# Optimization experiments

Measured on AMD Instinct MI355X. Metric: run time of the kernel, lower is better.

## Reference

```python
import jax, jax.numpy as jnp
import numpy as np

D_MODEL = 512
NUM_HEADS = 8
D_K = D_MODEL // NUM_HEADS
B, L = 2, 4096


def setup_inputs() -> dict:
    key = jax.random.key(0)
    ks = jax.random.split(key, 11)
    s = 1.0 / np.sqrt(D_MODEL)
    return {
        "Q": jax.random.normal(ks[0], (B, L, D_MODEL), jnp.float32),
        "K": jax.random.normal(ks[1], (B, L, D_MODEL), jnp.float32),
        "V": jax.random.normal(ks[2], (B, L, D_MODEL), jnp.float32),
        "Wq": jax.random.normal(ks[3], (D_MODEL, D_MODEL), jnp.float32) * s,
        "bq": jax.random.normal(ks[4], (D_MODEL,), jnp.float32) * s,
        "Wk": jax.random.normal(ks[5], (D_MODEL, D_MODEL), jnp.float32) * s,
        "bk": jax.random.normal(ks[6], (D_MODEL,), jnp.float32) * s,
        "Wv": jax.random.normal(ks[7], (D_MODEL, D_MODEL), jnp.float32) * s,
        "bv": jax.random.normal(ks[8], (D_MODEL,), jnp.float32) * s,
        "Wo": jax.random.normal(ks[9], (D_MODEL, D_MODEL), jnp.float32) * s,
        "bo": jax.random.normal(ks[10], (D_MODEL,), jnp.float32) * s,
    }


def reference(Q, K, V, Wq, bq, Wk, bk, Wv, bv, Wo, bo):
    b, l, d = Q.shape
    h, dk = NUM_HEADS, D_K
    # projections: [B, L, D] -> [B, H, L, dk]
    def proj(x, W, bias):
        y = x @ W.T + bias
        return y.reshape(b, l, h, dk).transpose(0, 2, 1, 3)
    q = proj(Q, Wq, bq)
    k = proj(K, Wk, bk)
    v = proj(V, Wv, bv)
    scores = jnp.einsum("bhqd,bhkd->bhqk", q, k) / jnp.sqrt(jnp.float32(dk))
    attn = jax.nn.softmax(scores, axis=-1)
    head_out = jnp.einsum("bhqk,bhkd->bhqd", attn, v)
    out = head_out.transpose(0, 2, 1, 3).reshape(b, l, d)
    return out @ Wo.T + bo
```

## Files before the change

### kernel.cpp

```cpp
#include <hip/hip_runtime.h>
#include <hip/hip_bf16.h>

#define SEQ 4096
#define DM 512
#define DK 64
#define NT (SEQ / 64)

typedef __attribute__((ext_vector_type(8))) short bf16x8;
typedef __attribute__((ext_vector_type(4))) short bf16x4;
typedef __attribute__((ext_vector_type(4))) float f32x4;

#define QSCL 0.18033688011112043f

static __device__ __forceinline__ short bf16h(float f) {
    union { __hip_bfloat16 h; short s; } u;
    u.h = __float2bfloat16(f);
    return u.s;
}

static __device__ __forceinline__ float fexp2(float x) {
#if __has_builtin(__builtin_amdgcn_exp2f)
    return __builtin_amdgcn_exp2f(x);
#else
    return exp2f(x);
#endif
}

static __device__ __forceinline__ void cvt16(const float* __restrict__ p, short* dst) {
    float4 a = *(const float4*)p;
    float4 b = *(const float4*)(p + 4);
    float4 e = *(const float4*)(p + 8);
    float4 d = *(const float4*)(p + 12);
    bf16x8 x0, x1;
    x0[0] = bf16h(a.x); x0[1] = bf16h(a.y); x0[2] = bf16h(a.z); x0[3] = bf16h(a.w);
    x0[4] = bf16h(b.x); x0[5] = bf16h(b.y); x0[6] = bf16h(b.z); x0[7] = bf16h(b.w);
    x1[0] = bf16h(e.x); x1[1] = bf16h(e.y); x1[2] = bf16h(e.z); x1[3] = bf16h(e.w);
    x1[4] = bf16h(d.x); x1[5] = bf16h(d.y); x1[6] = bf16h(d.z); x1[7] = bf16h(d.w);
    *(bf16x8*)dst = x0;
    *(bf16x8*)(dst + 8) = x1;
}

__global__ __launch_bounds__(256) void proj_qkv(
        const float* __restrict__ Qx, const float* __restrict__ Kx, const float* __restrict__ Vx,
        const float* __restrict__ Wq, const float* __restrict__ Wk, const float* __restrict__ Wv,
        const float* __restrict__ bq, const float* __restrict__ bk, const float* __restrict__ bv,
        short* __restrict__ qo, short* __restrict__ ko, short* __restrict__ vo) {
    __shared__ short Xs[64][72];
    __shared__ short Ws[64][72];
    const int z = blockIdx.z;
    const float* X    = z == 0 ? Qx : z == 1 ? Kx : Vx;
    const float* W    = z == 0 ? Wq : z == 1 ? Wk : Wv;
    const float* bias = z == 0 ? bq : z == 1 ? bk : bv;

    const int t = threadIdx.x, lane = t & 63, w = t >> 6;
    const int g = lane >> 4, c = lane & 15;
    const int sr = t >> 2, sc = t & 3;
    const int m0 = blockIdx.x << 6, n0 = blockIdx.y << 6;

    f32x4 acc[4] = {};
    const float* px = X + (size_t)(m0 + sr) * DM + sc * 16;
    const float* pw = W + (size_t)(n0 + sr) * DM + sc * 16;

    for (int k0 = 0; k0 < DM; k0 += 64) {
        cvt16(px, &Xs[sr][sc * 16]);
        cvt16(pw, &Ws[sr][sc * 16]);
        px += 64; pw += 64;
        __syncthreads();
        #pragma unroll
        for (int kc = 0; kc < 2; ++kc) {
            bf16x8 a8 = *(bf16x8*)&Xs[16 * w + c][32 * kc + 8 * g];
            #pragma unroll
            for (int f = 0; f < 4; ++f) {
                bf16x8 b8 = *(bf16x8*)&Ws[16 * f + c][32 * kc + 8 * g];
                acc[f] = __builtin_amdgcn_mfma_f32_16x16x32_bf16(a8, b8, acc[f], 0, 0, 0);
            }
        }
        __syncthreads();
    }

    float bs[4];
    #pragma unroll
    for (int f = 0; f < 4; ++f) bs[f] = bias[n0 + 16 * f + c];
    const int b = m0 >> 12, h = blockIdx.y;

    if (z == 0 || z == 1) {
        short* Yp = z == 0 ? qo : ko;
        const float scl = z == 0 ? QSCL : 1.0f;
        #pragma unroll
        for (int f = 0; f < 4; ++f) {
            #pragma unroll
            for (int r = 0; r < 4; ++r) {
                int m = m0 + 16 * w + 4 * g + r;
                Yp[((size_t)(b * 8 + h) * SEQ + (m & 4095)) * DK + 16 * f + c] =
                    bf16h((acc[f][r] + bs[f]) * scl);
            }
        }
    } else {
        short (&Ls)[64][72] = Xs;
        #pragma unroll
        for (int f = 0; f < 4; ++f) {
            #pragma unroll
            for (int r = 0; r < 4; ++r)
                Ls[16 * f + c][16 * w + 4 * g + r] = bf16h(acc[f][r] + bs[f]);
        }
        __syncthreads();
        bf16x8 r0 = *(bf16x8*)&Ls[sr][sc * 16];
        bf16x8 r1 = *(bf16x8*)&Ls[sr][sc * 16 + 8];
        short* dst = vo + ((size_t)(b * 8 + h) * DK + sr) * SEQ + (m0 & 4095) + sc * 16;
        *(bf16x8*)dst = r0;
        *(bf16x8*)(dst + 8) = r1;
    }
}

__global__ __launch_bounds__(256) void proj_out(const short* __restrict__ Xb,
        const float* __restrict__ W, const float* __restrict__ bias, float* __restrict__ Y) {
    __shared__ short Xs[64][72];
    __shared__ short Ws[64][72];
    const int t = threadIdx.x, lane = t & 63, w = t >> 6;
    const int g = lane >> 4, c = lane & 15;
    const int sr = t >> 2, sc = t & 3;
    const int m0 = blockIdx.x << 6, n0 = blockIdx.y << 6;

    f32x4 acc[4] = {};
    const short* px = Xb + (size_t)(m0 + sr) * DM + sc * 16;
    const float* pw = W + (size_t)(n0 + sr) * DM + sc * 16;

    for (int k0 = 0; k0 < DM; k0 += 64) {
        *(bf16x8*)&Xs[sr][sc * 16]     = *(const bf16x8*)px;
        *(bf16x8*)&Xs[sr][sc * 16 + 8] = *(const bf16x8*)(px + 8);
        cvt16(pw, &Ws[sr][sc * 16]);
        px += 64; pw += 64;
        __syncthreads();
        #pragma unroll
        for (int kc = 0; kc < 2; ++kc) {
            bf16x8 a8 = *(bf16x8*)&Xs[16 * w + c][32 * kc + 8 * g];
            #pragma unroll
            for (int f = 0; f < 4; ++f) {
                bf16x8 b8 = *(bf16x8*)&Ws[16 * f + c][32 * kc + 8 * g];
                acc[f] = __builtin_amdgcn_mfma_f32_16x16x32_bf16(a8, b8, acc[f], 0, 0, 0);
            }
        }
        __syncthreads();
    }

    #pragma unroll
    for (int f = 0; f < 4; ++f) {
        float bs = bias[n0 + 16 * f + c];
        #pragma unroll
        for (int r = 0; r < 4; ++r) {
            int m = m0 + 16 * w + 4 * g + r;
            Y[(size_t)m * DM + n0 + 16 * f + c] = acc[f][r] + bs;
        }
    }
}

__global__ __launch_bounds__(256) void attn_fwd(const short* __restrict__ qp,
        const short* __restrict__ kp, const short* __restrict__ vtp, short* __restrict__ ho) {
    __shared__ short Ks[64][72];
    __shared__ short Vts[64][76];
    const int t = threadIdx.x, lane = t & 63, w = t >> 6;
    const int g = lane >> 4, c = lane & 15;
    const int sr = t >> 2, sc = t & 3;
    const int q0 = blockIdx.x << 6, bh = blockIdx.y;

    const short* qrow = qp + ((size_t)bh * SEQ + q0 + 16 * w + c) * DK;
    const bf16x8 qf0 = *(const bf16x8*)(qrow + 8 * g);
    const bf16x8 qf1 = *(const bf16x8*)(qrow + 32 + 8 * g);

    f32x4 o4[4] = {};
    float m_run = -3.0e38f, l_run = 0.f;

    const short* kptr = kp + (size_t)bh * SEQ * DK + (size_t)sr * DK + sc * 16;
    const short* vptr = vtp + (size_t)bh * DK * SEQ + (size_t)sr * SEQ + sc * 16;
    bf16x8 kr0 = *(const bf16x8*)kptr;
    bf16x8 kr1 = *(const bf16x8*)(kptr + 8);
    bf16x8 vr0 = *(const bf16x8*)vptr;
    bf16x8 vr1 = *(const bf16x8*)(vptr + 8);

    for (int kt = 0; kt < NT; ++kt) {
        *(bf16x8*)&Ks[sr][sc * 16]     = kr0;
        *(bf16x8*)&Ks[sr][sc * 16 + 8] = kr1;
        {
            bf16x4 t0 = {vr0[0], vr0[1], vr0[2], vr0[3]};
            bf16x4 t1 = {vr0[4], vr0[5], vr0[6], vr0[7]};
            bf16x4 t2 = {vr1[0], vr1[1], vr1[2], vr1[3]};
            bf16x4 t3 = {vr1[4], vr1[5], vr1[6], vr1[7]};
            *(bf16x4*)&Vts[sr][sc * 16]      = t0;
            *(bf16x4*)&Vts[sr][sc * 16 + 4]  = t1;
            *(bf16x4*)&Vts[sr][sc * 16 + 8]  = t2;
            *(bf16x4*)&Vts[sr][sc * 16 + 12] = t3;
        }
        __syncthreads();
        if (kt + 1 < NT) {
            kptr += 64 * DK;
            vptr += 64;
            kr0 = *(const bf16x8*)kptr;
            kr1 = *(const bf16x8*)(kptr + 8);
            vr0 = *(const bf16x8*)vptr;
            vr1 = *(const bf16x8*)(vptr + 8);
        }

        f32x4 s4[4] = {};
        #pragma unroll
        for (int f = 0; f < 4; ++f) {
            bf16x8 a8 = *(bf16x8*)&Ks[16 * f + c][8 * g];
            s4[f] = __builtin_amdgcn_mfma_f32_16x16x32_bf16(a8, qf0, s4[f], 0, 0, 0);
        }
        #pragma unroll
        for (int f = 0; f < 4; ++f) {
            bf16x8 a8 = *(bf16x8*)&Ks[16 * f + c][32 + 8 * g];
            s4[f] = __builtin_amdgcn_mfma_f32_16x16x32_bf16(a8, qf1, s4[f], 0, 0, 0);
        }

        float pm = s4[0][0];
        #pragma unroll
        for (int f = 0; f < 4; ++f) {
            #pragma unroll
            for (int r = 0; r < 4; ++r) pm = fmaxf(pm, s4[f][r]);
        }
        pm = fmaxf(pm, __shfl_xor(pm, 16));
        pm = fmaxf(pm, __shfl_xor(pm, 32));

        if (__any(pm > m_run + 8.0f)) {
            float mnew  = fmaxf(m_run, pm);
            float alpha = fexp2(m_run - mnew);
            l_run *= alpha;
            #pragma unroll
            for (int fd = 0; fd < 4; ++fd) {
                #pragma unroll
                for (int r = 0; r < 4; ++r) o4[fd][r] *= alpha;
            }
            m_run = mnew;
        }

        float rs = 0.f;
        #pragma unroll
        for (int f = 0; f < 4; ++f) {
            #pragma unroll
            for (int r = 0; r < 4; ++r) {
                float p = fexp2(s4[f][r] - m_run);
                s4[f][r] = p;
                rs += p;
            }
        }
        rs += __shfl_xor(rs, 16);
        rs += __shfl_xor(rs, 32);
        l_run += rs;

        #pragma unroll
        for (int f = 0; f < 4; ++f) {
            bf16x4 pb = { bf16h(s4[f][0]), bf16h(s4[f][1]), bf16h(s4[f][2]), bf16h(s4[f][3]) };
            #pragma unroll
            for (int fd = 0; fd < 4; ++fd) {
                bf16x4 va = *(bf16x4*)&Vts[16 * fd + c][16 * f + 4 * g];
                o4[fd] = __builtin_amdgcn_mfma_f32_16x16x16bf16_1k(va, pb, o4[fd], 0, 0, 0);
            }
        }
        __syncthreads();
    }

    const float inv = 1.0f / l_run;
    short (&Ls)[64][72] = Ks;
    #pragma unroll
    for (int fd = 0; fd < 4; ++fd) {
        #pragma unroll
        for (int r = 0; r < 4; ++r)
            Ls[16 * w + c][16 * fd + 4 * g + r] = bf16h(o4[fd][r] * inv);
    }
    __syncthreads();
    const int b = bh >> 3, h = bh & 7;
    bf16x8 r0 = *(bf16x8*)&Ls[sr][sc * 16];
    bf16x8 r1 = *(bf16x8*)&Ls[sr][sc * 16 + 8];
    short* dst = ho + ((size_t)(b * SEQ + q0 + sr)) * DM + h * DK + sc * 16;
    *(bf16x8*)dst = r0;
    *(bf16x8*)(dst + 8) = r1;
}

extern "C" void kernel_launch(void* const* d_in, const int* in_sizes, int n_in,
                              void* d_out, int out_size, void* d_ws, size_t ws_size,
                              hipStream_t stream) {
    const float* Q  = (const float*)d_in[0];
    const float* K  = (const float*)d_in[1];
    const float* V  = (const float*)d_in[2];
    const float* Wq = (const float*)d_in[3];
    const float* bq = (const float*)d_in[4];
    const float* Wk = (const float*)d_in[5];
    const float* bk = (const float*)d_in[6];
    const float* Wv = (const float*)d_in[7];
    const float* bv = (const float*)d_in[8];
    const float* Wo = (const float*)d_in[9];
    const float* bo = (const float*)d_in[10];

    const size_t NIN = (size_t)2 * SEQ * DM;

    short* qws  = (short*)d_ws;
    short* kws  = qws + NIN;
    short* vtws = kws + NIN;
    short* hws  = vtws + NIN;

    proj_qkv<<<dim3(128, 8, 3), 256, 0, stream>>>(Q, K, V, Wq, Wk, Wv, bq, bk, bv,
                                                  qws, kws, vtws);
    attn_fwd<<<dim3(SEQ / 64, 16), 256, 0, stream>>>(qws, kws, vtws, hws);
    proj_out<<<dim3(128, 8), 256, 0, stream>>>(hws, Wo, bo, (float*)d_out);
}
```

Before: 293.0 us.

## Enlarge projection GEMM tiles to 128x128 and prefetch next K-slice into registers

Both projection kernels move from 64x64 tiles with 256 threads to 128x128 tiles with 512 threads, and each wave now computes a 64x32 sub-tile (4x2 MFMAs) to get more reuse per LDS load. The global loads for the next K slice are issued into registers before the current slice's MFMAs, overlapping memory latency with compute. The V-transpose epilogue is reworked for the wider tile. In exchange, the grid shrinks (768 and 256 blocks) and register pressure rises, which may reduce occupancy and leave CUs idle for proj_out.

```diff
diff --git a/kernel.cpp b/kernel.cpp
--- a/kernel.cpp
+++ b/kernel.cpp
@@ -26,11 +26,8 @@
 #endif
 }
 
-static __device__ __forceinline__ void cvt16(const float* __restrict__ p, short* dst) {
-    float4 a = *(const float4*)p;
-    float4 b = *(const float4*)(p + 4);
-    float4 e = *(const float4*)(p + 8);
-    float4 d = *(const float4*)(p + 12);
+static __device__ __forceinline__ void cvt16r(float4 a, float4 b, float4 e, float4 d,
+                                              short* dst) {
     bf16x8 x0, x1;
     x0[0] = bf16h(a.x); x0[1] = bf16h(a.y); x0[2] = bf16h(a.z); x0[3] = bf16h(a.w);
     x0[4] = bf16h(b.x); x0[5] = bf16h(b.y); x0[6] = bf16h(b.z); x0[7] = bf16h(b.w);
@@ -40,13 +37,14 @@
     *(bf16x8*)(dst + 8) = x1;
 }
 
-__global__ __launch_bounds__(256) void proj_qkv(
+__global__ __launch_bounds__(512) void proj_qkv(
         const float* __restrict__ Qx, const float* __restrict__ Kx, const float* __restrict__ Vx,
         const float* __restrict__ Wq, const float* __restrict__ Wk, const float* __restrict__ Wv,
         const float* __restrict__ bq, const float* __restrict__ bk, const float* __restrict__ bv,
         short* __restrict__ qo, short* __restrict__ ko, short* __restrict__ vo) {
-    __shared__ short Xs[64][72];
-    __shared__ short Ws[64][72];
+    __shared__ short lds[2][128][72];
+    short (*As)[72] = lds[0];
+    short (*Bs)[72] = lds[1];
     const int z = blockIdx.z;
     const float* X    = z == 0 ? Qx : z == 1 ? Kx : Vx;
     const float* W    = z == 0 ? Wq : z == 1 ? Wk : Wv;
@@ -54,103 +52,147 @@
 
     const int t = threadIdx.x, lane = t & 63, w = t >> 6;
     const int g = lane >> 4, c = lane & 15;
-    const int sr = t >> 2, sc = t & 3;
-    const int m0 = blockIdx.x << 6, n0 = blockIdx.y << 6;
-
-    f32x4 acc[4] = {};
-    const float* px = X + (size_t)(m0 + sr) * DM + sc * 16;
-    const float* pw = W + (size_t)(n0 + sr) * DM + sc * 16;
-
-    for (int k0 = 0; k0 < DM; k0 += 64) {
-        cvt16(px, &Xs[sr][sc * 16]);
-        cvt16(pw, &Ws[sr][sc * 16]);
-        px += 64; pw += 64;
-        __syncthreads();
+    const int wr = w >> 2, wc = w & 3;
+    const int row = t >> 2, sc = t & 3;
+    const int m0 = blockIdx.x << 7, n0 = blockIdx.y << 7;
+
+    f32x4 acc[4][2] = {};
+    const float* px = X + (size_t)(m0 + row) * DM + sc * 16;
+    const float* pw = W + (size_t)(n0 + row) * DM + sc * 16;
+
+    float4 x0 = *(const float4*)px,       x1 = *(const float4*)(px + 4),
+           x2 = *(const float4*)(px + 8), x3 = *(const float4*)(px + 12);
+    float4 w0 = *(const float4*)pw,       w1 = *(const float4*)(pw + 4),
+           w2 = *(const float4*)(pw + 8), w3 = *(const float4*)(pw + 12);
+
+    for (int kt = 0; kt < DM / 64; ++kt) {
+        cvt16r(x0, x1, x2, x3, &As[row][sc * 16]);
+        cvt16r(w0, w1, w2, w3, &Bs[row][sc * 16]);
+        __syncthreads();
+        if (kt + 1 < DM / 64) {
+            px += 64; pw += 64;
+            x0 = *(const float4*)px;       x1 = *(const float4*)(px + 4);
+            x2 = *(const float4*)(px + 8); x3 = *(const float4*)(px + 12);
+            w0 = *(const float4*)pw;       w1 = *(const float4*)(pw + 4);
+            w2 = *(const float4*)(pw + 8); w3 = *(const float4*)(pw + 12);
+        }
         #pragma unroll
         for (int kc = 0; kc < 2; ++kc) {
-            bf16x8 a8 = *(bf16x8*)&Xs[16 * w + c][32 * kc + 8 * g];
-            #pragma unroll
-            for (int f = 0; f < 4; ++f) {
-                bf16x8 b8 = *(bf16x8*)&Ws[16 * f + c][32 * kc + 8 * g];
-                acc[f] = __builtin_amdgcn_mfma_f32_16x16x32_bf16(a8, b8, acc[f], 0, 0, 0);
-            }
-        }
-        __syncthreads();
-    }
-
-    float bs[4];
-    #pragma unroll
-    for (int f = 0; f < 4; ++f) bs[f] = bias[n0 + 16 * f + c];
-    const int b = m0 >> 12, h = blockIdx.y;
-
-    if (z == 0 || z == 1) {
+            bf16x8 a8[4], b8[2];
+            #pragma unroll
+            for (int i = 0; i < 4; ++i)
+                a8[i] = *(bf16x8*)&As[wr * 64 + i * 16 + c][kc * 32 + 8 * g];
+            #pragma unroll
+            for (int j = 0; j < 2; ++j)
+                b8[j] = *(bf16x8*)&Bs[wc * 32 + j * 16 + c][kc * 32 + 8 * g];
+            #pragma unroll
+            for (int i = 0; i < 4; ++i)
+                #pragma unroll
+                for (int j = 0; j < 2; ++j)
+                    acc[i][j] = __builtin_amdgcn_mfma_f32_16x16x32_bf16(a8[i], b8[j], acc[i][j], 0, 0, 0);
+        }
+        __syncthreads();
+    }
+
+    const int b = m0 >> 12;
+    if (z != 2) {
         short* Yp = z == 0 ? qo : ko;
         const float scl = z == 0 ? QSCL : 1.0f;
         #pragma unroll
-        for (int f = 0; f < 4; ++f) {
-            #pragma unroll
-            for (int r = 0; r < 4; ++r) {
-                int m = m0 + 16 * w + 4 * g + r;
-                Yp[((size_t)(b * 8 + h) * SEQ + (m & 4095)) * DK + 16 * f + c] =
-                    bf16h((acc[f][r] + bs[f]) * scl);
-            }
+        for (int j = 0; j < 2; ++j) {
+            const int n = n0 + wc * 32 + j * 16 + c;
+            const float bsj = bias[n];
+            const int h = n >> 6, d = n & 63;
+            short* base = Yp + ((size_t)(b * 8 + h) * SEQ) * DK + d;
+            #pragma unroll
+            for (int i = 0; i < 4; ++i)
+                #pragma unroll
+                for (int r = 0; r < 4; ++r) {
+                    const int m = m0 + wr * 64 + i * 16 + 4 * g + r;
+                    base[(size_t)(m & 4095) * DK] = bf16h((acc[i][j][r] + bsj) * scl);
+                }
         }
     } else {
-        short (&Ls)[64][72] = Xs;
-        #pragma unroll
-        for (int f = 0; f < 4; ++f) {
-            #pragma unroll
-            for (int r = 0; r < 4; ++r)
-                Ls[16 * f + c][16 * w + 4 * g + r] = bf16h(acc[f][r] + bs[f]);
-        }
-        __syncthreads();
-        bf16x8 r0 = *(bf16x8*)&Ls[sr][sc * 16];
-        bf16x8 r1 = *(bf16x8*)&Ls[sr][sc * 16 + 8];
-        short* dst = vo + ((size_t)(b * 8 + h) * DK + sr) * SEQ + (m0 & 4095) + sc * 16;
-        *(bf16x8*)dst = r0;
-        *(bf16x8*)(dst + 8) = r1;
-    }
-}
-
-__global__ __launch_bounds__(256) void proj_out(const short* __restrict__ Xb,
+        short* L = &lds[0][0][0];
+        #pragma unroll
+        for (int j = 0; j < 2; ++j) {
+            const int nl = wc * 32 + j * 16 + c;
+            const float bsj = bias[n0 + nl];
+            #pragma unroll
+            for (int i = 0; i < 4; ++i)
+                #pragma unroll
+                for (int r = 0; r < 4; ++r)
+                    L[nl * 136 + wr * 64 + i * 16 + 4 * g + r] = bf16h(acc[i][j][r] + bsj);
+        }
+        __syncthreads();
+        const int rrow = t >> 2, q = t & 3;
+        const int n = n0 + rrow, h = n >> 6, d = n & 63;
+        short* dst = vo + ((size_t)(b * 8 + h) * DK + d) * SEQ + (m0 & 4095) + q * 32;
+        #pragma unroll
+        for (int k = 0; k < 4; ++k)
+            *(bf16x8*)(dst + 8 * k) = *(bf16x8*)&L[rrow * 136 + q * 32 + 8 * k];
+    }
+}
+
+__global__ __launch_bounds__(512) void proj_out(const short* __restrict__ Xb,
         const float* __restrict__ W, const float* __restrict__ bias, float* __restrict__ Y) {
-    __shared__ short Xs[64][72];
-    __shared__ short Ws[64][72];
+    __shared__ short lds[2][128][72];
+    short (*As)[72] = lds[0];
+    short (*Bs)[72] = lds[1];
     const int t = threadIdx.x, lane = t & 63, w = t >> 6;
     const int g = lane >> 4, c = lane & 15;
-    const int sr = t >> 2, sc = t & 3;
-    const int m0 = blockIdx.x << 6, n0 = blockIdx.y << 6;
-
-    f32x4 acc[4] = {};
-    const short* px = Xb + (size_t)(m0 + sr) * DM + sc * 16;
-    const float* pw = W + (size_t)(n0 + sr) * DM + sc * 16;
-
-    for (int k0 = 0; k0 < DM; k0 += 64) {
-        *(bf16x8*)&Xs[sr][sc * 16]     = *(const bf16x8*)px;
-        *(bf16x8*)&Xs[sr][sc * 16 + 8] = *(const bf16x8*)(px + 8);
-        cvt16(pw, &Ws[sr][sc * 16]);
-        px += 64; pw += 64;
-        __syncthreads();
+    const int wr = w >> 2, wc = w & 3;
+    const int row = t >> 2, sc = t & 3;
+    const int m0 = blockIdx.x << 7, n0 = blockIdx.y << 7;
+
+    f32x4 acc[4][2] = {};
+    const short* px = Xb + (size_t)(m0 + row) * DM + sc * 16;
+    const float* pw = W + (size_t)(n0 + row) * DM + sc * 16;
+
+    bf16x8 xb0 = *(const bf16x8*)px, xb1 = *(const bf16x8*)(px + 8);
+    float4 w0 = *(const float4*)pw,       w1 = *(const float4*)(pw + 4),
+           w2 = *(const float4*)(pw + 8), w3 = *(const float4*)(pw + 12);
+
+    for (int kt = 0; kt < DM / 64; ++kt) {
+        *(bf16x8*)&As[row][sc * 16]     = xb0;
+        *(bf16x8*)&As[row][sc * 16 + 8] = xb1;
+        cvt16r(w0, w1, w2, w3, &Bs[row][sc * 16]);
+        __syncthreads();
+        if (kt + 1 < DM / 64) {
+            px += 64; pw += 64;
+            xb0 = *(const bf16x8*)px; xb1 = *(const bf16x8*)(px + 8);
+            w0 = *(const float4*)pw;       w1 = *(const float4*)(pw + 4);
+            w2 = *(const float4*)(pw + 8); w3 = *(const float4*)(pw + 12);
+        }
         #pragma unroll
         for (int kc = 0; kc < 2; ++kc) {
-            bf16x8 a8 = *(bf16x8*)&Xs[16 * w + c][32 * kc + 8 * g];
-            #pragma unroll
-            for (int f = 0; f < 4; ++f) {
-                bf16x8 b8 = *(bf16x8*)&Ws[16 * f + c][32 * kc + 8 * g];
-                acc[f] = __builtin_amdgcn_mfma_f32_16x16x32_bf16(a8, b8, acc[f], 0, 0, 0);
+            bf16x8 a8[4], b8[2];
+            #pragma unroll
+            for (int i = 0; i < 4; ++i)
+                a8[i] = *(bf16x8*)&As[wr * 64 + i * 16 + c][kc * 32 + 8 * g];
+            #pragma unroll
+            for (int j = 0; j < 2; ++j)
+                b8[j] = *(bf16x8*)&Bs[wc * 32 + j * 16 + c][kc * 32 + 8 * g];
+            #pragma unroll
+            for (int i = 0; i < 4; ++i)
+                #pragma unroll
+                for (int j = 0; j < 2; ++j)
+                    acc[i][j] = __builtin_amdgcn_mfma_f32_16x16x32_bf16(a8[i], b8[j], acc[i][j], 0, 0, 0);
+        }
+        __syncthreads();
+    }
+
+    #pragma unroll
+    for (int j = 0; j < 2; ++j) {
+        const int n = n0 + wc * 32 + j * 16 + c;
+        const float bsj = bias[n];
+        #pragma unroll
+        for (int i = 0; i < 4; ++i)
+            #pragma unroll
+            for (int r = 0; r < 4; ++r) {
+                const int m = m0 + wr * 64 + i * 16 + 4 * g + r;
+                Y[(size_t)m * DM + n] = acc[i][j][r] + bsj;
             }
-        }
-        __syncthreads();
-    }
-
-    #pragma unroll
-    for (int f = 0; f < 4; ++f) {
-        float bs = bias[n0 + 16 * f + c];
-        #pragma unroll
-        for (int r = 0; r < 4; ++r) {
-            int m = m0 + 16 * w + 4 * g + r;
-            Y[(size_t)m * DM + n0 + 16 * f + c] = acc[f][r] + bs;
-        }
     }
 }
 
@@ -298,8 +340,8 @@
     short* vtws = kws + NIN;
     short* hws  = vtws + NIN;
 
-    proj_qkv<<<dim3(128, 8, 3), 256, 0, stream>>>(Q, K, V, Wq, Wk, Wv, bq, bk, bv,
-                                                  qws, kws, vtws);
+    proj_qkv<<<dim3(64, 4, 3), 512, 0, stream>>>(Q, K, V, Wq, Wk, Wv, bq, bk, bv,
+                                                 qws, kws, vtws);
     attn_fwd<<<dim3(SEQ / 64, 16), 256, 0, stream>>>(qws, kws, vtws, hws);
-    proj_out<<<dim3(128, 8), 256, 0, stream>>>(hws, Wo, bo, (float*)d_out);
-}
+    proj_out<<<dim3(64, 4), 512, 0, stream>>>(hws, Wo, bo, (float*)d_out);
+}
```

After: 284.2 us. 1.03x faster.
